# Kernel optimization log

Measured on AMD Instinct MI355X. Metric: run time of the kernel, lower is better.

Reference implementation:

```python
import jax, jax.numpy as jnp
import numpy as np

N, F_IN, F_OUT = 8192, 256, 256
NEG_BIG = jnp.float32(-9e15)


def setup_inputs() -> dict:
    key = jax.random.key(0)
    k1, k2, k3, k4 = jax.random.split(key, 4)
    h = jax.random.normal(k1, (N, F_IN), dtype=jnp.float32)
    adj = jax.random.randint(k2, (N, N), 0, 2, dtype=jnp.int32)
    # nn.Linear(in, out): weight [out, in], bias [out]
    lim = 1.0 / np.sqrt(F_IN)
    W = jax.random.uniform(k3, (F_OUT, F_IN), dtype=jnp.float32, minval=-lim, maxval=lim)
    b = jax.random.uniform(k4, (F_OUT,), dtype=jnp.float32, minval=-lim, maxval=lim)
    return {"h": h, "adj": adj, "W": W, "b": b}


def reference(h, adj, W, b):
    n = h.shape[0]
    scale = 1.0 / jnp.sqrt(jnp.asarray(h.shape[1], h.dtype))
    # attention = h @ h.T / sqrt(d)   -> [N, N]
    att = jnp.matmul(h, h.T) * scale
    # masked softmax over rows
    A = jax.nn.softmax(jnp.where(adj > 0, att, NEG_BIG), axis=1)
    eye = jnp.eye(n, dtype=A.dtype)
    A = (A + eye) * 0.5
    # first `k` rows overwritten with identity, k = count of nonzeros in adj[:, 0]
    k = jnp.sum(adj[:, 0] != 0)
    row_is_identity = jnp.arange(n)[:, None] < k  # [N, 1] broadcast mask
    A = jnp.where(row_is_identity, eye, A)
    h_new = jnp.matmul(h, W.T) + b
    return jax.nn.relu(jnp.matmul(A, h_new))
```

## Files before the change

kernel.cpp:

```cpp
#include <hip/hip_runtime.h>


typedef __attribute__((ext_vector_type(8))) short short8;
typedef __attribute__((ext_vector_type(4))) float f32x4;

#define NN 8192
#define DD 256
#define NEGB -1.2983e16f

__device__ __forceinline__ unsigned short f2bf(float f) {
  unsigned u = __builtin_bit_cast(unsigned, f);
  u += 0x7FFFu + ((u >> 16) & 1u);
  return (unsigned short)(u >> 16);
}
__device__ __forceinline__ float bf2f(unsigned short s) {
  unsigned u = ((unsigned)s) << 16;
  return __builtin_bit_cast(float, u);
}
__device__ __forceinline__ f32x4 mfma16(short8 a, short8 b, f32x4 c) {
  return __builtin_amdgcn_mfma_f32_16x16x32_bf16(a, b, c, 0, 0, 0);
}
__device__ __forceinline__ void gld16(const unsigned short* g, unsigned short* l) {
  __builtin_amdgcn_global_load_lds(
      (const __attribute__((address_space(1))) void*)g,
      (__attribute__((address_space(3))) void*)l, 16, 0, 0);
}

__global__ __launch_bounds__(256) void count_k(const int* __restrict__ adj,
                                               int* __restrict__ kout) {
  __shared__ int red[256];
  int gid = blockIdx.x * 256 + threadIdx.x;
  red[threadIdx.x] = (adj[(size_t)gid * NN] != 0);
  __syncthreads();
  for (int off = 128; off; off >>= 1) {
    if (threadIdx.x < off) red[threadIdx.x] += red[threadIdx.x + off];
    __syncthreads();
  }
  if (threadIdx.x == 0) atomicAdd(kout, red[0]);
}

__global__ __launch_bounds__(256) void conv_h(const float* __restrict__ h,
                                              unsigned short* __restrict__ hQf) {
  int gid = blockIdx.x * 256 + threadIdx.x;
  int i = gid >> 6, k4 = (gid & 63) * 4;
  float4 v = *(const float4*)(h + (size_t)i * DD + k4);
  size_t off = ((size_t)((i >> 4) * 8 + (k4 >> 5)) * 64 +
                (((k4 >> 3) & 3) * 16 + (i & 15))) * 8 + (k4 & 7);
  ushort4 o;
  o.x = f2bf(v.x); o.y = f2bf(v.y); o.z = f2bf(v.z); o.w = f2bf(v.w);
  *(ushort4*)(hQf + off) = o;
}

__global__ __launch_bounds__(256) void pack_wf(const float* __restrict__ W,
                                               unsigned short* __restrict__ Wf) {
  int gid = blockIdx.x * 256 + threadIdx.x;
  int l = gid & 63, f = gid >> 6, n16 = f >> 3, kk = f & 7;
  int lr = l & 15, lg = l >> 4;
  const float* src = W + (size_t)(n16 * 16 + lr) * DD + kk * 32 + lg * 8;
  float4 w0 = *(const float4*)src, w1 = *(const float4*)(src + 4);
  short8 o;
  o[0] = (short)f2bf(w0.x); o[1] = (short)f2bf(w0.y);
  o[2] = (short)f2bf(w0.z); o[3] = (short)f2bf(w0.w);
  o[4] = (short)f2bf(w1.x); o[5] = (short)f2bf(w1.y);
  o[6] = (short)f2bf(w1.z); o[7] = (short)f2bf(w1.w);
  *(short8*)(Wf + (size_t)gid * 8) = o;
}

__global__ __launch_bounds__(256) void hnew_k(const unsigned short* __restrict__ hQf,
                                              const unsigned short* __restrict__ Wf,
                                              const float* __restrict__ bias,
                                              unsigned short* __restrict__ hnb,
                                              unsigned short* __restrict__ hnV) {
  const int tid = threadIdx.x, w = tid >> 6, l = tid & 63, lr = l & 15, lg = l >> 4;
  const int row0 = blockIdx.x * 64 + w * 16;

  short8 a[8];
#pragma unroll
  for (int kk = 0; kk < 8; ++kk)
    a[kk] = *(const short8*)(hQf + ((size_t)((row0 >> 4) * 8 + kk) * 64 + l) * 8);

  f32x4 acc[16];
#pragma unroll
  for (int nt = 0; nt < 16; ++nt) acc[nt] = (f32x4){0.f, 0.f, 0.f, 0.f};

#pragma unroll
  for (int kk = 0; kk < 8; ++kk)
#pragma unroll
    for (int nt = 0; nt < 16; ++nt) {
      short8 bf = *(const short8*)(Wf + ((size_t)(nt * 8 + kk) * 64 + l) * 8);
      acc[nt] = mfma16(a[kk], bf, acc[nt]);
    }
#pragma unroll
  for (int nt = 0; nt < 16; ++nt) {
    const int col = nt * 16 + lr;
    const float bv = bias[col];
#pragma unroll
    for (int q = 0; q < 4; ++q) {
      const int row = row0 + lg * 4 + q;
      unsigned short r16 = f2bf(acc[nt][q] + bv);
      hnb[(size_t)row * DD + col] = r16;
      hnV[((size_t)((row >> 5) * 16 + nt) * 64 + ((row >> 3) & 3) * 16 + lr) * 8 +
          (row & 7)] = r16;
    }
  }
}

__global__ __launch_bounds__(256, 2) void attn_k(
    const unsigned short* __restrict__ hQf, const unsigned short* __restrict__ hnV,
    const int* __restrict__ adj, const int* __restrict__ kptr,
    float* __restrict__ pl, unsigned short* __restrict__ pO, int T) {
  __shared__ __align__(16) unsigned short sK[2][8192];
  __shared__ __align__(16) unsigned short sV[2][8192];
  __shared__ __align__(16) unsigned short sP[4][16][40];

  const int tid = threadIdx.x, w = tid >> 6, l = tid & 63, lr = l & 15, lg = l >> 4;
  const int ebx = (blockIdx.x + blockIdx.y) & 127;
  const int i0 = ebx * 64, c = blockIdx.y;
  const int kid = *kptr;
  if (i0 + 64 <= kid) return;

  const int r0 = i0 + w * 16;

  short8 qf[8];
#pragma unroll
  for (int kk = 0; kk < 8; ++kk)
    qf[kk] = *(const short8*)(hQf + ((size_t)((r0 >> 4) * 8 + kk) * 64 + l) * 8);

  f32x4 Oacc[16];
#pragma unroll
  for (int nt = 0; nt < 16; ++nt) Oacc[nt] = (f32x4){0.f, 0.f, 0.f, 0.f};
  float lsum[4] = {0.f, 0.f, 0.f, 0.f};
  const float c1 = 0.09016844005556021f;

  int arow[4];
#pragma unroll
  for (int q = 0; q < 4; ++q) arow[q] = (r0 + lg * 4 + q) * NN;

  const int jt0 = c * T;

  {
    const unsigned short* srcK = hQf + (size_t)jt0 * 8192;
    const unsigned short* srcV = hnV + (size_t)jt0 * 8192;
#pragma unroll
    for (int s = 0; s < 4; ++s) {
      const int so = (w * 4 + s) * 512;
      gld16(srcK + so + l * 8, &sK[0][so]);
      gld16(srcV + so + l * 8, &sV[0][so]);
    }
  }
  int avc[8], avn[8];
#pragma unroll
  for (int nt = 0; nt < 2; ++nt)
#pragma unroll
    for (int q = 0; q < 4; ++q)
      avc[nt * 4 + q] = adj[(size_t)arow[q] + jt0 * 32 + nt * 16 + lr];
  __syncthreads();

  for (int t = 0; t < T; ++t) {
    const int cur = t & 1;
    if (t + 1 < T) {
      const int jn = jt0 + t + 1;
      const unsigned short* srcK = hQf + (size_t)jn * 8192;
      const unsigned short* srcV = hnV + (size_t)jn * 8192;
#pragma unroll
      for (int s = 0; s < 4; ++s) {
        const int so = (w * 4 + s) * 512;
        gld16(srcK + so + l * 8, &sK[cur ^ 1][so]);
        gld16(srcV + so + l * 8, &sV[cur ^ 1][so]);
      }
#pragma unroll
      for (int nt = 0; nt < 2; ++nt)
#pragma unroll
        for (int q = 0; q < 4; ++q)
          avn[nt * 4 + q] = adj[(size_t)arow[q] + jn * 32 + nt * 16 + lr];
    }

    f32x4 S2[2];
    S2[0] = (f32x4){0.f, 0.f, 0.f, 0.f};
    S2[1] = (f32x4){0.f, 0.f, 0.f, 0.f};
#pragma unroll
    for (int kk = 0; kk < 8; ++kk)
#pragma unroll
      for (int nt = 0; nt < 2; ++nt) {
        short8 bf = *(const short8*)(&sK[cur][(nt * 8 + kk) * 512 + l * 8]);
        S2[nt] = mfma16(qf[kk], bf, S2[nt]);
      }

    float p0[4], p1[4];
#pragma unroll
    for (int q = 0; q < 4; ++q) {
      float sv0 = avc[q] ? fminf(S2[0][q] * c1, 60.f) : NEGB;
      float sv1 = avc[4 + q] ? fminf(S2[1][q] * c1, 60.f) : NEGB;
      p0[q] = __builtin_amdgcn_exp2f(sv0);
      p1[q] = __builtin_amdgcn_exp2f(sv1);
      lsum[q] += p0[q] + p1[q];
    }

#pragma unroll
    for (int q = 0; q < 4; ++q) {
      sP[w][lg * 4 + q][lr] = f2bf(p0[q]);
      sP[w][lg * 4 + q][16 + lr] = f2bf(p1[q]);
    }
    short8 pa = *(const short8*)(&sP[w][lr][lg * 8]);
#pragma unroll
    for (int cnt = 0; cnt < 16; ++cnt) {
      short8 vf = *(const short8*)(&sV[cur][cnt * 512 + l * 8]);
      Oacc[cnt] = mfma16(pa, vf, Oacc[cnt]);
    }

#pragma unroll
    for (int x = 0; x < 8; ++x) avc[x] = avn[x];
    __syncthreads();
  }

#pragma unroll
  for (int q = 0; q < 4; ++q) {
#pragma unroll
    for (int off = 1; off < 16; off <<= 1) lsum[q] += __shfl_xor(lsum[q], off);
    if (lr == 0) pl[(size_t)c * NN + r0 + lg * 4 + q] = lsum[q];
  }
#pragma unroll
  for (int cnt = 0; cnt < 16; ++cnt)
#pragma unroll
    for (int q = 0; q < 4; ++q) {
      int row = r0 + lg * 4 + q;
      pO[((size_t)c * NN + row) * DD + cnt * 16 + lr] = f2bf(Oacc[cnt][q]);
    }
}

__global__ __launch_bounds__(256) void comb_k(const float* __restrict__ pl,
                                              const unsigned short* __restrict__ pO,
                                              const unsigned short* __restrict__ hnb,
                                              const int* __restrict__ kptr,
                                              float* __restrict__ out, int S) {
  const int row = blockIdx.x, col = threadIdx.x;
  const int kid = *kptr;
  float v = bf2f(hnb[(size_t)row * DD + col]);
  float res;
  if (row < kid) {
    res = v;
  } else {
    float L = 0.f, acc = 0.f;
    for (int cc = 0; cc < S; ++cc) {
      L += pl[(size_t)cc * NN + row];
      acc += bf2f(pO[((size_t)cc * NN + row) * DD + col]);
    }
    res = acc * (0.5f / L) + 0.5f * v;
  }
  out[(size_t)row * DD + col] = fmaxf(res, 0.f);
}

extern "C" void kernel_launch(void* const* d_in, const int* in_sizes, int n_in,
                              void* d_out, int out_size, void* d_ws, size_t ws_size,
                              hipStream_t stream) {
  const float* h = (const float*)d_in[0];
  const int* adj = (const int*)d_in[1];
  const float* W = (const float*)d_in[2];
  const float* b = (const float*)d_in[3];
  float* out = (float*)d_out;

  char* ws = (char*)d_ws;
  const size_t MB4 = (size_t)NN * DD * 2;
  int* kbuf = (int*)ws;
  unsigned short* hQf = (unsigned short*)(ws + 256);
  unsigned short* hnb = (unsigned short*)(ws + 256 + MB4);
  unsigned short* hnV = (unsigned short*)(ws + 256 + 2 * MB4);
  unsigned short* Wf = (unsigned short*)(ws + 256 + 3 * MB4);
  char* dyn = ws + 256 + 3 * MB4 + (256 << 10);

  size_t fixed = 256 + 3 * MB4 + (256 << 10);
  int S = 16;
  while (S > 1 && fixed + (size_t)S * NN * (DD * 2 + 4) > ws_size) S >>= 1;
  const int T = 256 / S;

  float* pl = (float*)dyn;
  unsigned short* pO = (unsigned short*)(pl + (size_t)S * NN);

  hipMemsetAsync(kbuf, 0, 4, stream);
  hipLaunchKernelGGL(count_k, dim3(32), dim3(256), 0, stream, adj, kbuf);
  hipLaunchKernelGGL(conv_h, dim3(2048), dim3(256), 0, stream, h, hQf);
  hipLaunchKernelGGL(pack_wf, dim3(32), dim3(256), 0, stream, W, Wf);
  hipLaunchKernelGGL(hnew_k, dim3(NN / 64), dim3(256), 0, stream, hQf, Wf, b, hnb, hnV);
  hipLaunchKernelGGL(attn_k, dim3(NN / 64, S), dim3(256), 0, stream,
                     hQf, hnV, adj, kbuf, pl, pO, T);
  hipLaunchKernelGGL(comb_k, dim3(NN), dim3(256), 0, stream, pl, pO, hnb, kbuf, out, S);
}
```

Baseline: 131.4 us.

## Unroll attention loop by two, reorder grid, vectorize combine kernel

The attention loop is unrolled by two, so the double-buffer index and the adjacency register swap become compile-time constants and the per-iteration register copy goes away. The attention grid is transposed so the split index is blockIdx.x, which changes which blocks are scheduled together. The combine kernel now handles four columns per thread with vector loads and stores, launching a quarter as many blocks. Unrolling by two assumes T is even, which holds for the power-of-two split sizes except T=256 when S=1 is still even.

```diff
diff --git a/kernel.cpp b/kernel.cpp
--- a/kernel.cpp
+++ b/kernel.cpp
@@ -114,8 +114,8 @@
   __shared__ __align__(16) unsigned short sP[4][16][40];
 
   const int tid = threadIdx.x, w = tid >> 6, l = tid & 63, lr = l & 15, lg = l >> 4;
-  const int ebx = (blockIdx.x + blockIdx.y) & 127;
-  const int i0 = ebx * 64, c = blockIdx.y;
+  const int c = blockIdx.x, ty = blockIdx.y;
+  const int i0 = ty * 64;
   const int kid = *kptr;
   if (i0 + 64 <= kid) return;
 
@@ -148,70 +148,63 @@
       gld16(srcV + so + l * 8, &sV[0][so]);
     }
   }
-  int avc[8], avn[8];
+  int avA[8], avB[8];
 #pragma unroll
   for (int nt = 0; nt < 2; ++nt)
 #pragma unroll
     for (int q = 0; q < 4; ++q)
-      avc[nt * 4 + q] = adj[(size_t)arow[q] + jt0 * 32 + nt * 16 + lr];
+      avA[nt * 4 + q] = adj[(size_t)arow[q] + jt0 * 32 + nt * 16 + lr];
   __syncthreads();
 
-  for (int t = 0; t < T; ++t) {
-    const int cur = t & 1;
-    if (t + 1 < T) {
-      const int jn = jt0 + t + 1;
-      const unsigned short* srcK = hQf + (size_t)jn * 8192;
-      const unsigned short* srcV = hnV + (size_t)jn * 8192;
-#pragma unroll
-      for (int s = 0; s < 4; ++s) {
-        const int so = (w * 4 + s) * 512;
-        gld16(srcK + so + l * 8, &sK[cur ^ 1][so]);
-        gld16(srcV + so + l * 8, &sV[cur ^ 1][so]);
-      }
-#pragma unroll
-      for (int nt = 0; nt < 2; ++nt)
-#pragma unroll
-        for (int q = 0; q < 4; ++q)
-          avn[nt * 4 + q] = adj[(size_t)arow[q] + jn * 32 + nt * 16 + lr];
-    }
-
-    f32x4 S2[2];
-    S2[0] = (f32x4){0.f, 0.f, 0.f, 0.f};
-    S2[1] = (f32x4){0.f, 0.f, 0.f, 0.f};
-#pragma unroll
-    for (int kk = 0; kk < 8; ++kk)
-#pragma unroll
-      for (int nt = 0; nt < 2; ++nt) {
-        short8 bf = *(const short8*)(&sK[cur][(nt * 8 + kk) * 512 + l * 8]);
-        S2[nt] = mfma16(qf[kk], bf, S2[nt]);
-      }
-
-    float p0[4], p1[4];
-#pragma unroll
-    for (int q = 0; q < 4; ++q) {
-      float sv0 = avc[q] ? fminf(S2[0][q] * c1, 60.f) : NEGB;
-      float sv1 = avc[4 + q] ? fminf(S2[1][q] * c1, 60.f) : NEGB;
-      p0[q] = __builtin_amdgcn_exp2f(sv0);
-      p1[q] = __builtin_amdgcn_exp2f(sv1);
-      lsum[q] += p0[q] + p1[q];
-    }
-
-#pragma unroll
-    for (int q = 0; q < 4; ++q) {
-      sP[w][lg * 4 + q][lr] = f2bf(p0[q]);
-      sP[w][lg * 4 + q][16 + lr] = f2bf(p1[q]);
-    }
-    short8 pa = *(const short8*)(&sP[w][lr][lg * 8]);
-#pragma unroll
-    for (int cnt = 0; cnt < 16; ++cnt) {
-      short8 vf = *(const short8*)(&sV[cur][cnt * 512 + l * 8]);
-      Oacc[cnt] = mfma16(pa, vf, Oacc[cnt]);
-    }
-
-#pragma unroll
-    for (int x = 0; x < 8; ++x) avc[x] = avn[x];
-    __syncthreads();
-  }
+#define ATTN_ITER(T_IDX, CUR, MC, MN)                                          \
+  {                                                                            \
+    const int t_ = (T_IDX);                                                    \
+    if (t_ + 1 < T) {    \
+      const int jn = jt0 + t_ + 1;                                             \
+      const unsigned short* srcK = hQf + (size_t)jn * 8192;                    \
+      const unsigned short* srcV = hnV + (size_t)jn * 8192;                    \
+      _Pragma("unroll") for (int s = 0; s < 4; ++s) {                          \
+        const int so = (w * 4 + s) * 512;                                      \
+        gld16(srcK + so + l * 8, &sK[(CUR) ^ 1][so]);                          \
+        gld16(srcV + so + l * 8, &sV[(CUR) ^ 1][so]);                          \
+      }                                                                        \
+      _Pragma("unroll") for (int nt = 0; nt < 2; ++nt)                         \
+        _Pragma("unroll") for (int q = 0; q < 4; ++q)                          \
+          MN[nt * 4 + q] = adj[(size_t)arow[q] + jn * 32 + nt * 16 + lr];      \
+    }                                                                          \
+    f32x4 S2[2];                                                               \
+    S2[0] = (f32x4){0.f, 0.f, 0.f, 0.f};                                       \
+    S2[1] = (f32x4){0.f, 0.f, 0.f, 0.f};                                       \
+    _Pragma("unroll") for (int kk = 0; kk < 8; ++kk)                           \
+      _Pragma("unroll") for (int nt = 0; nt < 2; ++nt) {                       \
+        short8 bf = *(const short8*)(&sK[(CUR)][(nt * 8 + kk) * 512 + l * 8]); \
+        S2[nt] = mfma16(qf[kk], bf, S2[nt]);                                   \
+      }                                                                        \
+    float p0[4], p1[4];                                                        \
+    _Pragma("unroll") for (int q = 0; q < 4; ++q) {                            \
+      float sv0 = MC[q] ? fminf(S2[0][q] * c1, 60.f) : NEGB;                   \
+      float sv1 = MC[4 + q] ? fminf(S2[1][q] * c1, 60.f) : NEGB;               \
+      p0[q] = __builtin_amdgcn_exp2f(sv0);                                     \
+      p1[q] = __builtin_amdgcn_exp2f(sv1);                                     \
+      lsum[q] += p0[q] + p1[q];                                                \
+    }                                                                          \
+    _Pragma("unroll") for (int q = 0; q < 4; ++q) {                            \
+      sP[w][lg * 4 + q][lr] = f2bf(p0[q]);                                     \
+      sP[w][lg * 4 + q][16 + lr] = f2bf(p1[q]);                                \
+    }                                                                          \
+    short8 pa = *(const short8*)(&sP[w][lr][lg * 8]);                          \
+    _Pragma("unroll") for (int cnt = 0; cnt < 16; ++cnt) {                     \
+      short8 vf = *(const short8*)(&sV[(CUR)][cnt * 512 + l * 8]);             \
+      Oacc[cnt] = mfma16(pa, vf, Oacc[cnt]);                                   \
+    }                                                                          \
+    __syncthreads();                                                           \
+  }
+
+  for (int tt = 0; tt < T; tt += 2) {
+    ATTN_ITER(tt, 0, avA, avB);
+    ATTN_ITER(tt + 1, 1, avB, avA);
+  }
+#undef ATTN_ITER
 
 #pragma unroll
   for (int q = 0; q < 4; ++q) {
@@ -233,21 +226,28 @@
                                               const unsigned short* __restrict__ hnb,
                                               const int* __restrict__ kptr,
                                               float* __restrict__ out, int S) {
-  const int row = blockIdx.x, col = threadIdx.x;
+  const int row = blockIdx.x * 4 + (threadIdx.x >> 6);
+  const int col = (threadIdx.x & 63) * 4;
   const int kid = *kptr;
-  float v = bf2f(hnb[(size_t)row * DD + col]);
-  float res;
+  ushort4 hv = *(const ushort4*)(hnb + (size_t)row * DD + col);
+  float v0 = bf2f(hv.x), v1 = bf2f(hv.y), v2 = bf2f(hv.z), v3 = bf2f(hv.w);
+  float4 r;
   if (row < kid) {
-    res = v;
+    r.x = v0; r.y = v1; r.z = v2; r.w = v3;
   } else {
-    float L = 0.f, acc = 0.f;
+    float L = 0.f, a0 = 0.f, a1 = 0.f, a2 = 0.f, a3 = 0.f;
     for (int cc = 0; cc < S; ++cc) {
       L += pl[(size_t)cc * NN + row];
-      acc += bf2f(pO[((size_t)cc * NN + row) * DD + col]);
-    }
-    res = acc * (0.5f / L) + 0.5f * v;
-  }
-  out[(size_t)row * DD + col] = fmaxf(res, 0.f);
+      ushort4 ov = *(const ushort4*)(pO + ((size_t)cc * NN + row) * DD + col);
+      a0 += bf2f(ov.x); a1 += bf2f(ov.y); a2 += bf2f(ov.z); a3 += bf2f(ov.w);
+    }
+    float inv = 0.5f / L;
+    r.x = a0 * inv + 0.5f * v0; r.y = a1 * inv + 0.5f * v1;
+    r.z = a2 * inv + 0.5f * v2; r.w = a3 * inv + 0.5f * v3;
+  }
+  r.x = fmaxf(r.x, 0.f); r.y = fmaxf(r.y, 0.f);
+  r.z = fmaxf(r.z, 0.f); r.w = fmaxf(r.w, 0.f);
+  *(float4*)(out + (size_t)row * DD + col) = r;
 }
 
 extern "C" void kernel_launch(void* const* d_in, const int* in_sizes, int n_in,
@@ -281,7 +281,7 @@
   hipLaunchKernelGGL(conv_h, dim3(2048), dim3(256), 0, stream, h, hQf);
   hipLaunchKernelGGL(pack_wf, dim3(32), dim3(256), 0, stream, W, Wf);
   hipLaunchKernelGGL(hnew_k, dim3(NN / 64), dim3(256), 0, stream, hQf, Wf, b, hnb, hnV);
-  hipLaunchKernelGGL(attn_k, dim3(NN / 64, S), dim3(256), 0, stream,
+  hipLaunchKernelGGL(attn_k, dim3(S, NN / 64), dim3(256), 0, stream,
                      hQf, hnV, adj, kbuf, pl, pO, T);
-  hipLaunchKernelGGL(comb_k, dim3(NN), dim3(256), 0, stream, pl, pO, hnb, kbuf, out, S);
-}
+  hipLaunchKernelGGL(comb_k, dim3(NN / 4), dim3(256), 0, stream, pl, pO, hnb, kbuf, out, S);
+}
```

New measurement: 117.5 us. -10.6%, faster.

## Fuse prep kernels, double attention row tile, vectorize combine and hnew stores

Applied to the files above, without the earlier changes.

Merges the count, h-conversion and W-packing kernels into one launch. The attention kernel now gives each wave 32 rows instead of 16, so every K/V tile loaded into LDS feeds twice as many MFMAs. The grid is reordered so split-index blocks sharing rows are adjacent. The adj prefetch across iterations is replaced by a load inside each iteration, which may expose load latency. The combine kernel and the hnV stores now use vector loads and stores; the larger attention tile raises register pressure and halves the block count.

```diff
diff --git a/kernel.cpp b/kernel.cpp
--- a/kernel.cpp
+++ b/kernel.cpp
@@ -26,44 +26,45 @@
       (__attribute__((address_space(3))) void*)l, 16, 0, 0);
 }
 
-__global__ __launch_bounds__(256) void count_k(const int* __restrict__ adj,
-                                               int* __restrict__ kout) {
-  __shared__ int red[256];
-  int gid = blockIdx.x * 256 + threadIdx.x;
-  red[threadIdx.x] = (adj[(size_t)gid * NN] != 0);
-  __syncthreads();
-  for (int off = 128; off; off >>= 1) {
-    if (threadIdx.x < off) red[threadIdx.x] += red[threadIdx.x + off];
+__global__ __launch_bounds__(256) void prep_k(const float* __restrict__ h,
+                                              const float* __restrict__ W,
+                                              const int* __restrict__ adj,
+                                              unsigned short* __restrict__ hQf,
+                                              unsigned short* __restrict__ Wf,
+                                              int* __restrict__ kout) {
+  const int bx = blockIdx.x, tid = threadIdx.x;
+  if (bx < 2048) {
+    int gid = bx * 256 + tid;
+    int i = gid >> 6, k4 = (gid & 63) * 4;
+    float4 v = *(const float4*)(h + (size_t)i * DD + k4);
+    size_t off = ((size_t)((i >> 4) * 8 + (k4 >> 5)) * 64 +
+                  (((k4 >> 3) & 3) * 16 + (i & 15))) * 8 + (k4 & 7);
+    ushort4 o;
+    o.x = f2bf(v.x); o.y = f2bf(v.y); o.z = f2bf(v.z); o.w = f2bf(v.w);
+    *(ushort4*)(hQf + off) = o;
+  } else if (bx < 2080) {
+    __shared__ int red[256];
+    int gid = (bx - 2048) * 256 + tid;
+    red[tid] = (adj[(size_t)gid * NN] != 0);
     __syncthreads();
-  }
-  if (threadIdx.x == 0) atomicAdd(kout, red[0]);
-}
-
-__global__ __launch_bounds__(256) void conv_h(const float* __restrict__ h,
-                                              unsigned short* __restrict__ hQf) {
-  int gid = blockIdx.x * 256 + threadIdx.x;
-  int i = gid >> 6, k4 = (gid & 63) * 4;
-  float4 v = *(const float4*)(h + (size_t)i * DD + k4);
-  size_t off = ((size_t)((i >> 4) * 8 + (k4 >> 5)) * 64 +
-                (((k4 >> 3) & 3) * 16 + (i & 15))) * 8 + (k4 & 7);
-  ushort4 o;
-  o.x = f2bf(v.x); o.y = f2bf(v.y); o.z = f2bf(v.z); o.w = f2bf(v.w);
-  *(ushort4*)(hQf + off) = o;
-}
-
-__global__ __launch_bounds__(256) void pack_wf(const float* __restrict__ W,
-                                               unsigned short* __restrict__ Wf) {
-  int gid = blockIdx.x * 256 + threadIdx.x;
-  int l = gid & 63, f = gid >> 6, n16 = f >> 3, kk = f & 7;
-  int lr = l & 15, lg = l >> 4;
-  const float* src = W + (size_t)(n16 * 16 + lr) * DD + kk * 32 + lg * 8;
-  float4 w0 = *(const float4*)src, w1 = *(const float4*)(src + 4);
-  short8 o;
-  o[0] = (short)f2bf(w0.x); o[1] = (short)f2bf(w0.y);
-  o[2] = (short)f2bf(w0.z); o[3] = (short)f2bf(w0.w);
-  o[4] = (short)f2bf(w1.x); o[5] = (short)f2bf(w1.y);
-  o[6] = (short)f2bf(w1.z); o[7] = (short)f2bf(w1.w);
-  *(short8*)(Wf + (size_t)gid * 8) = o;
+    for (int off = 128; off; off >>= 1) {
+      if (tid < off) red[tid] += red[tid + off];
+      __syncthreads();
+    }
+    if (tid == 0) atomicAdd(kout, red[0]);
+  } else {
+    int gid = (bx - 2080) * 256 + tid;
+    int l = gid & 63, f = gid >> 6, n16 = f >> 3, kk = f & 7;
+    int lr = l & 15, lg = l >> 4;
+    const float* src = W + (size_t)(n16 * 16 + lr) * DD + kk * 32 + lg * 8;
+    float4 w0 = *(const float4*)src, w1 = *(const float4*)(src + 4);
+    short8 o;
+    o[0] = (short)f2bf(w0.x); o[1] = (short)f2bf(w0.y);
+    o[2] = (short)f2bf(w0.z); o[3] = (short)f2bf(w0.w);
+    o[4] = (short)f2bf(w1.x); o[5] = (short)f2bf(w1.y);
+    o[6] = (short)f2bf(w1.z); o[7] = (short)f2bf(w1.w);
+    *(short8*)(Wf + (size_t)gid * 8) = o;
+  }
 }
 
 __global__ __launch_bounds__(256) void hnew_k(const unsigned short* __restrict__ hQf,
@@ -90,18 +91,20 @@
       short8 bf = *(const short8*)(Wf + ((size_t)(nt * 8 + kk) * 64 + l) * 8);
       acc[nt] = mfma16(a[kk], bf, acc[nt]);
     }
+  const int rowbase = row0 + lg * 4;
 #pragma unroll
   for (int nt = 0; nt < 16; ++nt) {
     const int col = nt * 16 + lr;
     const float bv = bias[col];
-#pragma unroll
-    for (int q = 0; q < 4; ++q) {
-      const int row = row0 + lg * 4 + q;
-      unsigned short r16 = f2bf(acc[nt][q] + bv);
-      hnb[(size_t)row * DD + col] = r16;
-      hnV[((size_t)((row >> 5) * 16 + nt) * 64 + ((row >> 3) & 3) * 16 + lr) * 8 +
-          (row & 7)] = r16;
-    }
+    ushort4 o4;
+    unsigned short r16[4];
+#pragma unroll
+    for (int q = 0; q < 4; ++q) r16[q] = f2bf(acc[nt][q] + bv);
+    o4.x = r16[0]; o4.y = r16[1]; o4.z = r16[2]; o4.w = r16[3];
+#pragma unroll
+    for (int q = 0; q < 4; ++q) hnb[(size_t)(rowbase + q) * DD + col] = r16[q];
+    *(ushort4*)(hnV + ((size_t)((rowbase >> 5) * 16 + nt) * 64 +
+                       ((rowbase >> 3) & 3) * 16 + lr) * 8 + (rowbase & 7)) = o4;
   }
 }
 
@@ -111,30 +114,31 @@
     float* __restrict__ pl, unsigned short* __restrict__ pO, int T) {
   __shared__ __align__(16) unsigned short sK[2][8192];
   __shared__ __align__(16) unsigned short sV[2][8192];
-  __shared__ __align__(16) unsigned short sP[4][16][40];
+  __shared__ __align__(16) unsigned short sP[4][2][16][40];
 
   const int tid = threadIdx.x, w = tid >> 6, l = tid & 63, lr = l & 15, lg = l >> 4;
-  const int ebx = (blockIdx.x + blockIdx.y) & 127;
-  const int i0 = ebx * 64, c = blockIdx.y;
+  const int c = blockIdx.x, ty = blockIdx.y;
+  const int i0 = ty * 128;
   const int kid = *kptr;
-  if (i0 + 64 <= kid) return;
-
-  const int r0 = i0 + w * 16;
-
-  short8 qf[8];
-#pragma unroll
-  for (int kk = 0; kk < 8; ++kk)
-    qf[kk] = *(const short8*)(hQf + ((size_t)((r0 >> 4) * 8 + kk) * 64 + l) * 8);
-
-  f32x4 Oacc[16];
-#pragma unroll
-  for (int nt = 0; nt < 16; ++nt) Oacc[nt] = (f32x4){0.f, 0.f, 0.f, 0.f};
-  float lsum[4] = {0.f, 0.f, 0.f, 0.f};
+  if (i0 + 128 <= kid) return;
+
+  const int r0 = i0 + w * 32;
+
+  short8 qf[2][8];
+#pragma unroll
+  for (int rt = 0; rt < 2; ++rt)
+#pragma unroll
+    for (int kk = 0; kk < 8; ++kk)
+      qf[rt][kk] =
+          *(const short8*)(hQf + ((size_t)(((r0 >> 4) + rt) * 8 + kk) * 64 + l) * 8);
+
+  f32x4 Oacc[2][16];
+#pragma unroll
+  for (int rt = 0; rt < 2; ++rt)
+#pragma unroll
+    for (int nt = 0; nt < 16; ++nt) Oacc[rt][nt] = (f32x4){0.f, 0.f, 0.f, 0.f};
+  float lsum[2][4] = {{0.f, 0.f, 0.f, 0.f}, {0.f, 0.f, 0.f, 0.f}};
   const float c1 = 0.09016844005556021f;
-
-  int arow[4];
-#pragma unroll
-  for (int q = 0; q < 4; ++q) arow[q] = (r0 + lg * 4 + q) * NN;
 
   const int jt0 = c * T;
 
@@ -148,18 +152,24 @@
       gld16(srcV + so + l * 8, &sV[0][so]);
     }
   }
-  int avc[8], avn[8];
-#pragma unroll
-  for (int nt = 0; nt < 2; ++nt)
-#pragma unroll
-    for (int q = 0; q < 4; ++q)
-      avc[nt * 4 + q] = adj[(size_t)arow[q] + jt0 * 32 + nt * 16 + lr];
   __syncthreads();
 
   for (int t = 0; t < T; ++t) {
     const int cur = t & 1;
+    const int jt = jt0 + t;
+
+    int av[2][2][4];
+#pragma unroll
+    for (int rt = 0; rt < 2; ++rt)
+#pragma unroll
+      for (int nt = 0; nt < 2; ++nt)
+#pragma unroll
+        for (int q = 0; q < 4; ++q)
+          av[rt][nt][q] =
+              adj[(size_t)(r0 + rt * 16 + lg * 4 + q) * NN + jt * 32 + nt * 16 + lr];
+
     if (t + 1 < T) {
-      const int jn = jt0 + t + 1;
+      const int jn = jt + 1;
       const unsigned short* srcK = hQf + (size_t)jn * 8192;
       const unsigned short* srcV = hnV + (size_t)jn * 8192;
 #pragma unroll
@@ -168,64 +178,69 @@
         gld16(srcK + so + l * 8, &sK[cur ^ 1][so]);
         gld16(srcV + so + l * 8, &sV[cur ^ 1][so]);
       }
-#pragma unroll
-      for (int nt = 0; nt < 2; ++nt)
-#pragma unroll
-        for (int q = 0; q < 4; ++q)
-          avn[nt * 4 + q] = adj[(size_t)arow[q] + jn * 32 + nt * 16 + lr];
-    }
-
-    f32x4 S2[2];
-    S2[0] = (f32x4){0.f, 0.f, 0.f, 0.f};
-    S2[1] = (f32x4){0.f, 0.f, 0.f, 0.f};
+    }
+
+    f32x4 S2[2][2];
+#pragma unroll
+    for (int rt = 0; rt < 2; ++rt)
+#pragma unroll
+      for (int nt = 0; nt < 2; ++nt) S2[rt][nt] = (f32x4){0.f, 0.f, 0.f, 0.f};
 #pragma unroll
     for (int kk = 0; kk < 8; ++kk)
 #pragma unroll
       for (int nt = 0; nt < 2; ++nt) {
         short8 bf = *(const short8*)(&sK[cur][(nt * 8 + kk) * 512 + l * 8]);
-        S2[nt] = mfma16(qf[kk], bf, S2[nt]);
-      }
-
-    float p0[4], p1[4];
-#pragma unroll
-    for (int q = 0; q < 4; ++q) {
-      float sv0 = avc[q] ? fminf(S2[0][q] * c1, 60.f) : NEGB;
-      float sv1 = avc[4 + q] ? fminf(S2[1][q] * c1, 60.f) : NEGB;
-      p0[q] = __builtin_amdgcn_exp2f(sv0);
-      p1[q] = __builtin_amdgcn_exp2f(sv1);
-      lsum[q] += p0[q] + p1[q];
-    }
-
-#pragma unroll
-    for (int q = 0; q < 4; ++q) {
-      sP[w][lg * 4 + q][lr] = f2bf(p0[q]);
-      sP[w][lg * 4 + q][16 + lr] = f2bf(p1[q]);
-    }
-    short8 pa = *(const short8*)(&sP[w][lr][lg * 8]);
+        S2[0][nt] = mfma16(qf[0][kk], bf, S2[0][nt]);
+        S2[1][nt] = mfma16(qf[1][kk], bf, S2[1][nt]);
+      }
+
+#pragma unroll
+    for (int rt = 0; rt < 2; ++rt) {
+      float p0[4], p1[4];
+#pragma unroll
+      for (int q = 0; q < 4; ++q) {
+        float sv0 = av[rt][0][q] ? fminf(S2[rt][0][q] * c1, 60.f) : NEGB;
+        float sv1 = av[rt][1][q] ? fminf(S2[rt][1][q] * c1, 60.f) : NEGB;
+        p0[q] = __builtin_amdgcn_exp2f(sv0);
+        p1[q] = __builtin_amdgcn_exp2f(sv1);
+        lsum[rt][q] += p0[q] + p1[q];
+      }
+#pragma unroll
+      for (int q = 0; q < 4; ++q) {
+        sP[w][rt][lg * 4 + q][lr] = f2bf(p0[q]);
+        sP[w][rt][lg * 4 + q][16 + lr] = f2bf(p1[q]);
+      }
+    }
+
+    short8 pa0 = *(const short8*)(&sP[w][0][lr][lg * 8]);
+    short8 pa1 = *(const short8*)(&sP[w][1][lr][lg * 8]);
 #pragma unroll
     for (int cnt = 0; cnt < 16; ++cnt) {
       short8 vf = *(const short8*)(&sV[cur][cnt * 512 + l * 8]);
-      Oacc[cnt] = mfma16(pa, vf, Oacc[cnt]);
-    }
-
-#pragma unroll
-    for (int x = 0; x < 8; ++x) avc[x] = avn[x];
+      Oacc[0][cnt] = mfma16(pa0, vf, Oacc[0][cnt]);
+      Oacc[1][cnt] = mfma16(pa1, vf, Oacc[1][cnt]);
+    }
     __syncthreads();
   }
 
 #pragma unroll
-  for (int q = 0; q < 4; ++q) {
-#pragma unroll
-    for (int off = 1; off < 16; off <<= 1) lsum[q] += __shfl_xor(lsum[q], off);
-    if (lr == 0) pl[(size_t)c * NN + r0 + lg * 4 + q] = lsum[q];
-  }
+  for (int rt = 0; rt < 2; ++rt)
+#pragma unroll
+    for (int q = 0; q < 4; ++q) {
+      float s = lsum[rt][q];
+#pragma unroll
+      for (int off = 1; off < 16; off <<= 1) s += __shfl_xor(s, off);
+      if (lr == 0) pl[(size_t)c * NN + r0 + rt * 16 + lg * 4 + q] = s;
+    }
 #pragma unroll
   for (int cnt = 0; cnt < 16; ++cnt)
 #pragma unroll
-    for (int q = 0; q < 4; ++q) {
-      int row = r0 + lg * 4 + q;
-      pO[((size_t)c * NN + row) * DD + cnt * 16 + lr] = f2bf(Oacc[cnt][q]);
-    }
+    for (int rt = 0; rt < 2; ++rt)
+#pragma unroll
+      for (int q = 0; q < 4; ++q) {
+        int row = r0 + rt * 16 + lg * 4 + q;
+        pO[((size_t)c * NN + row) * DD + cnt * 16 + lr] = f2bf(Oacc[rt][cnt][q]);
+      }
 }
 
 __global__ __launch_bounds__(256) void comb_k(const float* __restrict__ pl,
@@ -233,21 +248,28 @@
                                               const unsigned short* __restrict__ hnb,
                                               const int* __restrict__ kptr,
                                               float* __restrict__ out, int S) {
-  const int row = blockIdx.x, col = threadIdx.x;
+  const int row = blockIdx.x * 4 + (threadIdx.x >> 6);
+  const int col = (threadIdx.x & 63) * 4;
   const int kid = *kptr;
-  float v = bf2f(hnb[(size_t)row * DD + col]);
-  float res;
+  ushort4 hv = *(const ushort4*)(hnb + (size_t)row * DD + col);
+  float v0 = bf2f(hv.x), v1 = bf2f(hv.y), v2 = bf2f(hv.z), v3 = bf2f(hv.w);
+  float4 r;
   if (row < kid) {
-    res = v;
+    r.x = v0; r.y = v1; r.z = v2; r.w = v3;
   } else {
-    float L = 0.f, acc = 0.f;
+    float L = 0.f, a0 = 0.f, a1 = 0.f, a2 = 0.f, a3 = 0.f;
     for (int cc = 0; cc < S; ++cc) {
       L += pl[(size_t)cc * NN + row];
-      acc += bf2f(pO[((size_t)cc * NN + row) * DD + col]);
-    }
-    res = acc * (0.5f / L) + 0.5f * v;
-  }
-  out[(size_t)row * DD + col] = fmaxf(res, 0.f);
+      ushort4 ov = *(const ushort4*)(pO + ((size_t)cc * NN + row) * DD + col);
+      a0 += bf2f(ov.x); a1 += bf2f(ov.y); a2 += bf2f(ov.z); a3 += bf2f(ov.w);
+    }
+    float inv = 0.5f / L;
+    r.x = a0 * inv + 0.5f * v0; r.y = a1 * inv + 0.5f * v1;
+    r.z = a2 * inv + 0.5f * v2; r.w = a3 * inv + 0.5f * v3;
+  }
+  r.x = fmaxf(r.x, 0.f); r.y = fmaxf(r.y, 0.f);
+  r.z = fmaxf(r.z, 0.f); r.w = fmaxf(r.w, 0.f);
+  *(float4*)(out + (size_t)row * DD + col) = r;
 }
 
 extern "C" void kernel_launch(void* const* d_in, const int* in_sizes, int n_in,
@@ -277,11 +299,9 @@
   unsigned short* pO = (unsigned short*)(pl + (size_t)S * NN);
 
   hipMemsetAsync(kbuf, 0, 4, stream);
-  hipLaunchKernelGGL(count_k, dim3(32), dim3(256), 0, stream, adj, kbuf);
-  hipLaunchKernelGGL(conv_h, dim3(2048), dim3(256), 0, stream, h, hQf);
-  hipLaunchKernelGGL(pack_wf, dim3(32), dim3(256), 0, stream, W, Wf);
+  hipLaunchKernelGGL(prep_k, dim3(2112), dim3(256), 0, stream, h, W, adj, hQf, Wf, kbuf);
   hipLaunchKernelGGL(hnew_k, dim3(NN / 64), dim3(256), 0, stream, hQf, Wf, b, hnb, hnV);
-  hipLaunchKernelGGL(attn_k, dim3(NN / 64, S), dim3(256), 0, stream,
+  hipLaunchKernelGGL(attn_k, dim3(S, NN / 128), dim3(256), 0, stream,
                      hQf, hnV, adj, kbuf, pl, pO, T);
-  hipLaunchKernelGGL(comb_k, dim3(NN), dim3(256), 0, stream, pl, pO, hnb, kbuf, out, S);
-}
+  hipLaunchKernelGGL(comb_k, dim3(NN / 4), dim3(256), 0, stream, pl, pO, hnb, kbuf, out, S);
+}
```

Measured after the change: 150.8 us. +14.7%, slower.
